# Kernel tuning notes

Measured on AMD Instinct MI355X. Metric: run time of the kernel, lower is better.

Reference implementation:

```python
import jax, jax.numpy as jnp
import numpy as np

B, D_IN, U, M = 8192, 512, 256, 50  # batch, input_size, num_units(=v_size), max_n_msgs


def _w(key, shape, scale=0.02):
    return (jax.random.normal(key, shape, dtype=jnp.float32) * scale)


def setup_inputs() -> dict:
    key = jax.random.key(0)
    ks = jax.random.split(key, 32)
    inp = {
        "X": jax.random.normal(ks[0], (B, D_IN), dtype=jnp.float32),
        "S": jax.random.normal(ks[1], (B, M, U), dtype=jnp.float32),
        "h": jax.random.normal(ks[2], (B, U), dtype=jnp.float32),
        "v": jax.random.normal(ks[3], (B, U), dtype=jnp.float32),
        # attention params
        "W_sa": _w(ks[4], (U, U)), "W_ha": _w(ks[5], (U, U)),
        "b_a": jnp.zeros((U,), jnp.float32), "v_a": _w(ks[6], (U,)),
        # gates
        "W_f": _w(ks[7], (U, U)), "W_hf": _w(ks[8], (U, U)), "b_f": jnp.zeros((U,), jnp.float32),
        "W_o": _w(ks[9], (U, U)), "W_ho": _w(ks[10], (U, U)), "b_o": jnp.zeros((U,), jnp.float32),
        "W_t": _w(ks[11], (U, U)), "W_ht": _w(ks[12], (U, U)), "b_t": jnp.zeros((U,), jnp.float32),
        "W_k": _w(ks[13], (D_IN, U)), "W_hk": _w(ks[14], (U, U)), "W_vk": _w(ks[15], (U, U)), "b_k": jnp.zeros((U,), jnp.float32),
        "W_s": _w(ks[16], (D_IN, U)), "W_hs": _w(ks[17], (U, U)), "b_s": jnp.zeros((U,), jnp.float32),
        "W_v": _w(ks[18], (U, U)), "W_hv": _w(ks[19], (U, U)), "b_v": jnp.zeros((U,), jnp.float32),
    }
    return inp


def reference(X, S, h, v,
              W_sa, W_ha, b_a, v_a,
              W_f, W_hf, b_f,
              W_o, W_ho, b_o,
              W_t, W_ht, b_t,
              W_k, W_hk, W_vk, b_k,
              W_s, W_hs, b_s,
              W_v, W_hv, b_v):
    # additive attention over messages: a [B, M, U]
    a = jnp.tanh(jnp.einsum('bmv,vu->bmu', S, W_sa) + (h @ W_ha + b_a)[:, None, :])
    scores = jnp.einsum('bmu,u->bm', a, v_a)            # [B, M]
    P = jax.nn.softmax(scores, axis=1)                  # [B, M]
    text = jnp.einsum('bm,bmv->bv', P, S)               # [B, U]
    # LSTM-like gates
    F = jax.nn.sigmoid(text @ W_f + h @ W_hf + b_f)
    O = jax.nn.sigmoid(text @ W_o + h @ W_ho + b_o)
    text_new = jnp.tanh(text @ W_t + h @ W_ht + b_t)
    V = F * v + O * text_new                            # [B, U]
    k = jax.nn.sigmoid(X @ W_k + h @ W_hk + V @ W_vk + b_k)
    hx = jnp.tanh(X @ W_s + h @ W_hs + b_s)
    hv = jnp.tanh(V @ W_v + h @ W_hv + b_v)
    H = (1.0 - k) * hv + k * hx                         # [B, U]
    # original returns (H, P, MSINStateTuple(H, V)); new_state.h == H
    return (H, P, V)
```

## Files before the change

### kernel.cpp

```cpp
#include <hip/hip_runtime.h>
#include <cstddef>

typedef __bf16 bf16x8 __attribute__((ext_vector_type(8)));
typedef unsigned short u16x8 __attribute__((ext_vector_type(8)));
typedef float f32x4 __attribute__((ext_vector_type(4)));

#define B_N 8192
#define M_N 50
#define R_N (B_N * M_N)
#define P_OFF ((size_t)B_N * 256)
#define V_OFF ((size_t)B_N * 256 + (size_t)B_N * 50)

__device__ __forceinline__ float bf2f(unsigned short u) {
  return __uint_as_float(((unsigned int)u) << 16);
}
__device__ __forceinline__ unsigned short f2bf(float f) {
  unsigned int u = __float_as_uint(f);
  u += 0x7fffu + ((u >> 16) & 1u);
  return (unsigned short)(u >> 16);
}
__device__ __forceinline__ float fsig(float x) { return 1.f / (1.f + __expf(-x)); }
__device__ __forceinline__ float ftanh(float x) {
  float e = __expf(2.f * x);
  return 1.f - 2.f / (e + 1.f);
}

__device__ __forceinline__ float ld_ext(const void* p, size_t i, bool f32) {
  return f32 ? ((const float*)p)[i] : bf2f(((const unsigned short*)p)[i]);
}

__device__ __forceinline__ void gload_lds16(const void* g, void* l) {
  __builtin_amdgcn_global_load_lds(
      (const __attribute__((address_space(1))) unsigned int*)g,
      (__attribute__((address_space(3))) unsigned int*)l, 16, 0, 0);
}

__device__ __forceinline__ unsigned swz(unsigned b) {
  return b ^ (((b >> 7) & 7u) << 4);
}

__global__ void probe_dtype(const void* __restrict__ X, int* __restrict__ flag) {
  const int lane = threadIdx.x;
  const unsigned short u = ((const unsigned short*)X)[lane * 2];
  const int e = (u >> 7) & 0xff;
  const bool plausible = (e >= 110 && e <= 144) || (u == 0);
  const unsigned long long m = __ballot(plausible);
  if (lane == 0) *flag = (__popcll(m) < 32) ? 1 : 0;
}

struct TJobs {
  const void* src[15];
  unsigned short* dst[15];
  int K[15];
};

__global__ __launch_bounds__(256) void transpose_weights(TJobs jobs, const int* __restrict__ flagp) {
  const bool f32 = *flagp != 0;
  const int z = blockIdx.z;
  const void* __restrict__ src = jobs.src[z];
  unsigned short* __restrict__ dst = jobs.dst[z];
  const int K = jobs.K[z];
  const int k0 = blockIdx.y * 16;
  if (k0 >= K) return;
  const int n0 = blockIdx.x * 16;
  __shared__ __align__(16) unsigned short tile[16][17];
  const int tx = threadIdx.x & 15, ty = threadIdx.x >> 4;
  const size_t sidx = (size_t)(k0 + ty) * 256 + n0 + tx;
  tile[ty][tx] = f32 ? f2bf(((const float*)src)[sidx]) : ((const unsigned short*)src)[sidx];
  __syncthreads();
  dst[(size_t)(n0 + ty) * K + k0 + tx] = tile[tx][ty];
}

struct GJob {
  const void* A[3];
  const unsigned short* Wt[3];
  int K[3];
  int atag[3];
  const void* bias;
  const unsigned short* add;
  unsigned short* out;
  int act;
};
struct GJobs { GJob j[4]; };

__global__ __launch_bounds__(256) void gemm_small(GJobs jobs, const int* __restrict__ flagp) {
  const bool flag32 = *flagp != 0;
  const GJob job = jobs.j[blockIdx.z];
  const int tid = threadIdx.x;
  const int row0 = blockIdx.x * 64;
  const int col0 = blockIdx.y * 128;
  __shared__ __align__(16) unsigned short As[2][64][40];
  __shared__ __align__(16) unsigned short Ws[2][128][40];

  f32x4 acc[2][4];
#pragma unroll
  for (int i = 0; i < 2; ++i)
#pragma unroll
    for (int j = 0; j < 4; ++j) acc[i][j] = (f32x4){0.f, 0.f, 0.f, 0.f};

  const int wave = tid >> 6, lane = tid & 63;
  const int wr = wave >> 1, wc = wave & 1;
  const int quad = lane >> 4, l16 = lane & 15;

  const void* Aseg[3]; const unsigned short* Wseg[3]; int Kseg[3]; bool Fseg[3];
  int nseg = 0, nt = 0, sbeg[4];
  sbeg[0] = 0;
  for (int p = 0; p < 3; ++p) {
    if (job.K[p] == 0) break;
    Aseg[nseg] = job.A[p]; Wseg[nseg] = job.Wt[p]; Kseg[nseg] = job.K[p];
    Fseg[nseg] = (job.atag[p] == 1) || (job.atag[p] == 2 && flag32);
    nt += job.K[p] / 32;
    ++nseg; sbeg[nseg] = nt;
  }

  const int rA = tid >> 2, cA = (tid & 3) * 8;
  const int rW = tid >> 2, cW = (tid & 3) * 8;

  uint4 pa, pw0, pw1;
  float4 fa, fb;
  bool pf32 = false;

  auto issue = [&](int t) {
    int s = 0;
    while (t >= sbeg[s + 1]) ++s;
    const int k0 = (t - sbeg[s]) * 32;
    const int Kp = Kseg[s];
    pf32 = Fseg[s];
    if (pf32) {
      const float* fp = (const float*)Aseg[s] + (size_t)(row0 + rA) * Kp + k0 + cA;
      fa = *(const float4*)fp;
      fb = *(const float4*)(fp + 4);
    } else {
      pa = *(const uint4*)((const unsigned short*)Aseg[s] + (size_t)(row0 + rA) * Kp + k0 + cA);
    }
    pw0 = *(const uint4*)&Wseg[s][(size_t)(col0 + rW) * Kp + k0 + cW];
    pw1 = *(const uint4*)&Wseg[s][(size_t)(col0 + rW + 64) * Kp + k0 + cW];
  };
  auto commit = [&](int buf) {
    if (pf32) {
      u16x8 v;
      v[0] = f2bf(fa.x); v[1] = f2bf(fa.y); v[2] = f2bf(fa.z); v[3] = f2bf(fa.w);
      v[4] = f2bf(fb.x); v[5] = f2bf(fb.y); v[6] = f2bf(fb.z); v[7] = f2bf(fb.w);
      *(u16x8*)&As[buf][rA][cA] = v;
    } else {
      *(uint4*)&As[buf][rA][cA] = pa;
    }
    *(uint4*)&Ws[buf][rW][cW] = pw0;
    *(uint4*)&Ws[buf][rW + 64][cW] = pw1;
  };

  issue(0);
  commit(0);
  __syncthreads();

  int buf = 0;
  for (int t = 0; t < nt; ++t) {
    if (t + 1 < nt) issue(t + 1);
    bf16x8 af[2], bfr[4];
#pragma unroll
    for (int mi = 0; mi < 2; ++mi)
      af[mi] = *(const bf16x8*)&As[buf][wr * 32 + mi * 16 + l16][quad * 8];
#pragma unroll
    for (int ni = 0; ni < 4; ++ni)
      bfr[ni] = *(const bf16x8*)&Ws[buf][wc * 64 + ni * 16 + l16][quad * 8];
#pragma unroll
    for (int mi = 0; mi < 2; ++mi)
#pragma unroll
      for (int ni = 0; ni < 4; ++ni)
        acc[mi][ni] = __builtin_amdgcn_mfma_f32_16x16x32_bf16(af[mi], bfr[ni], acc[mi][ni], 0, 0, 0);
    if (t + 1 < nt) commit(buf ^ 1);
    __syncthreads();
    buf ^= 1;
  }

#pragma unroll
  for (int mi = 0; mi < 2; ++mi) {
#pragma unroll
    for (int ni = 0; ni < 4; ++ni) {
      const int col = col0 + wc * 64 + ni * 16 + l16;
      const float bias = job.bias ? ld_ext(job.bias, col, flag32) : 0.f;
      const int rowb = row0 + wr * 32 + mi * 16 + quad * 4;
#pragma unroll
      for (int r = 0; r < 4; ++r) {
        float v = acc[mi][ni][r] + bias;
        const size_t idx = (size_t)(rowb + r) * 256 + col;
        if (job.add) v += bf2f(job.add[idx]);
        if (job.act == 1) v = fsig(v);
        else if (job.act == 2) v = ftanh(v);
        job.out[idx] = f2bf(v);
      }
    }
  }
}

__global__ __launch_bounds__(512, 4) void attn_scores(
    const void* __restrict__ S,
    const unsigned short* __restrict__ WsaT,
    const unsigned short* __restrict__ hWa,
    const void* __restrict__ v_a,
    float* __restrict__ scores,
    const int* __restrict__ flagp) {
  const bool f32 = *flagp != 0;
  const int tid = threadIdx.x;
  const int r0 = blockIdx.x * 128;

  __shared__ __align__(128) unsigned short As[2 * 128 * 32];
  __shared__ __align__(128) unsigned short Ws[2 * 256 * 32];
  __shared__ float hWs[4][256];
  __shared__ float vas[256];
  __shared__ __align__(16) float red[128][4];

  const int wave = tid >> 6, lane = tid & 63;
  const int wr = wave >> 2, wc = wave & 3;
  const int quad = lane >> 4, l16 = lane & 15;

  const unsigned oA = tid * 16;
  const unsigned lA = swz(oA);
  const unsigned rowA = lA >> 6, slA = (lA >> 4) & 3;
  const size_t gAbase = (size_t)(r0 + rowA) * 256 + slA * 8;
  const size_t gWbase0 = (size_t)rowA * 256 + slA * 8;
  const size_t gWbase1 = (size_t)(rowA + 128) * 256 + slA * 8;

  auto stage = [&](int buf, int k0) {
    char* const aDst = (char*)As + buf * 8192 + (wave << 10);
    char* const wDst0 = (char*)Ws + buf * 16384 + (wave << 10);
    char* const wDst1 = wDst0 + 8192;
    if (f32) {
      const float* fp = (const float*)S + gAbase + k0;
      const float4 a = *(const float4*)fp;
      const float4 b = *(const float4*)(fp + 4);
      u16x8 t;
      t[0] = f2bf(a.x); t[1] = f2bf(a.y); t[2] = f2bf(a.z); t[3] = f2bf(a.w);
      t[4] = f2bf(b.x); t[5] = f2bf(b.y); t[6] = f2bf(b.z); t[7] = f2bf(b.w);
      *(u16x8*)((char*)As + buf * 8192 + oA) = t;
    } else {
      gload_lds16((const unsigned short*)S + gAbase + k0, aDst);
    }
    gload_lds16(WsaT + gWbase0 + k0, wDst0);
    gload_lds16(WsaT + gWbase1 + k0, wDst1);
  };

  f32x4 acc[4][4];
#pragma unroll
  for (int i = 0; i < 4; ++i)
#pragma unroll
    for (int j = 0; j < 4; ++j) acc[i][j] = (f32x4){0.f, 0.f, 0.f, 0.f};

  stage(0, 0);
  const int b_first = r0 / 50;
  for (int i = tid; i < 1024; i += 512) {
    const int j = i >> 8, u = i & 255;
    const int b = b_first + j;
    hWs[j][u] = (b < B_N) ? bf2f(hWa[(size_t)b * 256 + u]) : 0.f;
  }
  if (tid < 256) vas[tid] = ld_ext(v_a, tid, f32);
  __syncthreads();

  int buf = 0;
  for (int t = 0; t < 8; ++t) {
    if (t < 7) stage(buf ^ 1, (t + 1) * 32);
    const char* aB = (const char*)As + buf * 8192;
    const char* wB = (const char*)Ws + buf * 16384;
    bf16x8 af[4], bfr[4];
#pragma unroll
    for (int mi = 0; mi < 4; ++mi) {
      const unsigned lb = (unsigned)(wr * 64 + mi * 16 + l16) * 64 + quad * 16;
      af[mi] = *(const bf16x8*)(aB + swz(lb));
    }
#pragma unroll
    for (int ni = 0; ni < 4; ++ni) {
      const unsigned lb = (unsigned)(wc * 64 + ni * 16 + l16) * 64 + quad * 16;
      bfr[ni] = *(const bf16x8*)(wB + swz(lb));
    }
#pragma unroll
    for (int mi = 0; mi < 4; ++mi)
#pragma unroll
      for (int ni = 0; ni < 4; ++ni)
        acc[mi][ni] = __builtin_amdgcn_mfma_f32_16x16x32_bf16(af[mi], bfr[ni], acc[mi][ni], 0, 0, 0);
    __syncthreads();
    buf ^= 1;
  }

  float ps[4][4];
#pragma unroll
  for (int mi = 0; mi < 4; ++mi) {
#pragma unroll
    for (int r = 0; r < 4; ++r) {
      const int rl = wr * 64 + mi * 16 + quad * 4 + r;
      const int bj = (r0 + rl) / 50 - b_first;
      float s = 0.f;
#pragma unroll
      for (int ni = 0; ni < 4; ++ni) {
        const int col = wc * 64 + ni * 16 + l16;
        s += ftanh(acc[mi][ni][r] + hWs[bj][col]) * vas[col];
      }
      ps[mi][r] = s;
    }
  }
#pragma unroll
  for (int mi = 0; mi < 4; ++mi)
#pragma unroll
    for (int r = 0; r < 4; ++r) {
      float v = ps[mi][r];
      v += __shfl_xor(v, 1);
      v += __shfl_xor(v, 2);
      v += __shfl_xor(v, 4);
      v += __shfl_xor(v, 8);
      if (l16 == 0) red[wr * 64 + mi * 16 + quad * 4 + r][wc] = v;
    }
  __syncthreads();
  if (tid < 128) {
    const float4 rr = *(const float4*)&red[tid][0];
    scores[r0 + tid] = rr.x + rr.y + rr.z + rr.w;
  }
}

__global__ __launch_bounds__(256) void softmax_text(
    const float* __restrict__ scores,
    const void* __restrict__ S,
    float* __restrict__ out,
    unsigned short* __restrict__ text,
    const int* __restrict__ flagp) {
  const bool f32 = *flagp != 0;
  const int tid = threadIdx.x;
  const int wave = tid >> 6, lane = tid & 63;
  const int b = blockIdx.x * 4 + wave;
  __shared__ float Pl[4][64];

  float s = (lane < 50) ? scores[(size_t)b * 50 + lane] : -1e30f;
  float mx = s;
#pragma unroll
  for (int off = 32; off > 0; off >>= 1) mx = fmaxf(mx, __shfl_xor(mx, off));
  float e = (lane < 50) ? __expf(s - mx) : 0.f;
  float sum = e;
#pragma unroll
  for (int off = 32; off > 0; off >>= 1) sum += __shfl_xor(sum, off);
  const float p = e / sum;
  if (lane < 50) out[P_OFF + (size_t)b * 50 + lane] = p;
  Pl[wave][lane] = p;
  __syncthreads();

  float a0 = 0.f, a1 = 0.f, a2 = 0.f, a3 = 0.f;
  const size_t base = (size_t)b * 50 * 256 + lane * 4;
  for (int m = 0; m < 50; ++m) {
    const float pm = Pl[wave][m];
    const size_t ix = base + (size_t)m * 256;
    float s0, s1, s2, s3;
    if (f32) {
      const float4 sv = *(const float4*)((const float*)S + ix);
      s0 = sv.x; s1 = sv.y; s2 = sv.z; s3 = sv.w;
    } else {
      const uint2 raw = *(const uint2*)((const unsigned short*)S + ix);
      s0 = bf2f((unsigned short)(raw.x & 0xffffu));
      s1 = bf2f((unsigned short)(raw.x >> 16));
      s2 = bf2f((unsigned short)(raw.y & 0xffffu));
      s3 = bf2f((unsigned short)(raw.y >> 16));
    }
    a0 += pm * s0; a1 += pm * s1; a2 += pm * s2; a3 += pm * s3;
  }
  uint2 o;
  o.x = (unsigned int)f2bf(a0) | ((unsigned int)f2bf(a1) << 16);
  o.y = (unsigned int)f2bf(a2) | ((unsigned int)f2bf(a3) << 16);
  *(uint2*)&text[(size_t)b * 256 + lane * 4] = o;
}

__global__ __launch_bounds__(256) void v_combine(
    const unsigned short* __restrict__ F, const unsigned short* __restrict__ O,
    const unsigned short* __restrict__ T,
    const void* __restrict__ v, float* __restrict__ out,
    const int* __restrict__ flagp) {
  const bool f32 = *flagp != 0;
  const int i = (blockIdx.x * 256 + threadIdx.x) * 4;
  float v0, v1, v2, v3;
  if (f32) {
    const float4 vv = *(const float4*)((const float*)v + i);
    v0 = vv.x; v1 = vv.y; v2 = vv.z; v3 = vv.w;
  } else {
    const uint2 vr = *(const uint2*)((const unsigned short*)v + i);
    v0 = bf2f((unsigned short)(vr.x & 0xffffu));
    v1 = bf2f((unsigned short)(vr.x >> 16));
    v2 = bf2f((unsigned short)(vr.y & 0xffffu));
    v3 = bf2f((unsigned short)(vr.y >> 16));
  }
  const uint2 Fr = *(const uint2*)&F[i];
  const uint2 Or = *(const uint2*)&O[i];
  const uint2 Tr = *(const uint2*)&T[i];
  float4 o;
  o.x = bf2f((unsigned short)(Fr.x & 0xffffu)) * v0 + bf2f((unsigned short)(Or.x & 0xffffu)) * bf2f((unsigned short)(Tr.x & 0xffffu));
  o.y = bf2f((unsigned short)(Fr.x >> 16))     * v1 + bf2f((unsigned short)(Or.x >> 16))     * bf2f((unsigned short)(Tr.x >> 16));
  o.z = bf2f((unsigned short)(Fr.y & 0xffffu)) * v2 + bf2f((unsigned short)(Or.y & 0xffffu)) * bf2f((unsigned short)(Tr.y & 0xffffu));
  o.w = bf2f((unsigned short)(Fr.y >> 16))     * v3 + bf2f((unsigned short)(Or.y >> 16))     * bf2f((unsigned short)(Tr.y >> 16));
  *(float4*)&out[V_OFF + i] = o;
}

__global__ __launch_bounds__(256) void h_combine(
    const unsigned short* __restrict__ kk, const unsigned short* __restrict__ hv,
    const unsigned short* __restrict__ hx, float* __restrict__ Hout) {
  const int i = (blockIdx.x * 256 + threadIdx.x) * 4;
  const uint2 kr = *(const uint2*)&kk[i];
  const uint2 vr = *(const uint2*)&hv[i];
  const uint2 xr = *(const uint2*)&hx[i];
  const float k0 = bf2f((unsigned short)(kr.x & 0xffffu)), k1 = bf2f((unsigned short)(kr.x >> 16));
  const float k2 = bf2f((unsigned short)(kr.y & 0xffffu)), k3 = bf2f((unsigned short)(kr.y >> 16));
  const float hv0 = bf2f((unsigned short)(vr.x & 0xffffu)), hv1 = bf2f((unsigned short)(vr.x >> 16));
  const float hv2 = bf2f((unsigned short)(vr.y & 0xffffu)), hv3 = bf2f((unsigned short)(vr.y >> 16));
  const float hx0 = bf2f((unsigned short)(xr.x & 0xffffu)), hx1 = bf2f((unsigned short)(xr.x >> 16));
  const float hx2 = bf2f((unsigned short)(xr.y & 0xffffu)), hx3 = bf2f((unsigned short)(xr.y >> 16));
  float4 o;
  o.x = (1.f - k0) * hv0 + k0 * hx0;
  o.y = (1.f - k1) * hv1 + k1 * hx1;
  o.z = (1.f - k2) * hv2 + k2 * hx2;
  o.w = (1.f - k3) * hv3 + k3 * hx3;
  *(float4*)&Hout[i] = o;
}

extern "C" void kernel_launch(void* const* d_in, const int* in_sizes, int n_in,
                              void* d_out, int out_size, void* d_ws, size_t ws_size,
                              hipStream_t stream) {
  const void* X   = d_in[0];
  const void* S   = d_in[1];
  const void* h   = d_in[2];
  const void* v   = d_in[3];
  const void* b_a = d_in[6];
  const void* v_a = d_in[7];
  const void* b_f = d_in[10];
  const void* b_o = d_in[13];
  const void* b_t = d_in[16];
  const void* b_k = d_in[20];
  const void* b_s = d_in[23];
  const void* b_v = d_in[26];

  float* out = (float*)d_out;
  float* out_V = out + V_OFF;

  char* ws = (char*)d_ws;
  int* flag = (int*)ws;
  size_t off = 256;

  const int widx[15] = {4, 5, 8, 9, 11, 12, 14, 15, 17, 18, 19, 21, 22, 24, 25};
  const int wK[15]   = {256, 256, 256, 256, 256, 256, 256, 256, 512, 256, 256, 512, 256, 256, 256};
  TJobs tj;
  unsigned short* wt[15];
  for (int i = 0; i < 15; ++i) {
    wt[i] = (unsigned short*)(ws + off);
    off += (size_t)wK[i] * 256 * 2;
    tj.src[i] = d_in[widx[i]];
    tj.dst[i] = wt[i];
    tj.K[i] = wK[i];
  }
  const unsigned short *WsaT = wt[0], *WhaT = wt[1], *WfT = wt[2], *WhfT = wt[3],
                       *WoT = wt[4], *WhoT = wt[5], *WtT = wt[6], *WhtT = wt[7],
                       *WkT = wt[8], *WhkT = wt[9], *WvkT = wt[10], *WsT = wt[11],
                       *WhsT = wt[12], *WvT = wt[13], *WhvT = wt[14];
  off = (off + 255) & ~(size_t)255;
  const size_t BS = (size_t)B_N * 256 * 2;
  unsigned short* hWa   = (unsigned short*)(ws + off); off += BS;
  float* scores         = (float*)(ws + off);          off += (size_t)R_N * sizeof(float);
  unsigned short* text  = (unsigned short*)(ws + off); off += BS;
  unsigned short* Fb    = (unsigned short*)(ws + off); off += BS;
  unsigned short* Ob    = (unsigned short*)(ws + off); off += BS;
  unsigned short* Tb    = (unsigned short*)(ws + off); off += BS;
  unsigned short* kpre  = (unsigned short*)(ws + off); off += BS;
  unsigned short* hx    = (unsigned short*)(ws + off); off += BS;
  unsigned short* hvpre = (unsigned short*)(ws + off); off += BS;

  probe_dtype<<<1, 64, 0, stream>>>(X, flag);
  transpose_weights<<<dim3(16, 32, 15), 256, 0, stream>>>(tj, flag);

  GJobs jA;
  for (int i = 0; i < 4; ++i) jA.j[i] = GJob{};
  jA.j[0].A[0] = h;  jA.j[0].atag[0] = 2; jA.j[0].Wt[0] = WhaT; jA.j[0].K[0] = 256;
  jA.j[0].bias = b_a; jA.j[0].out = hWa; jA.j[0].act = 0;
  jA.j[1].A[0] = X;  jA.j[1].atag[0] = 2; jA.j[1].Wt[0] = WkT;  jA.j[1].K[0] = 512;
  jA.j[1].A[1] = h;  jA.j[1].atag[1] = 2; jA.j[1].Wt[1] = WhkT; jA.j[1].K[1] = 256;
  jA.j[1].bias = b_k; jA.j[1].out = kpre; jA.j[1].act = 0;
  jA.j[2].A[0] = X;  jA.j[2].atag[0] = 2; jA.j[2].Wt[0] = WsT;  jA.j[2].K[0] = 512;
  jA.j[2].A[1] = h;  jA.j[2].atag[1] = 2; jA.j[2].Wt[1] = WhsT; jA.j[2].K[1] = 256;
  jA.j[2].bias = b_s; jA.j[2].out = hx; jA.j[2].act = 2;
  jA.j[3].A[0] = h;  jA.j[3].atag[0] = 2; jA.j[3].Wt[0] = WhvT; jA.j[3].K[0] = 256;
  jA.j[3].bias = b_v; jA.j[3].out = hvpre; jA.j[3].act = 0;
  gemm_small<<<dim3(128, 2, 4), 256, 0, stream>>>(jA, flag);

  attn_scores<<<dim3(R_N / 128), 512, 0, stream>>>(S, WsaT, hWa, v_a, scores, flag);
  softmax_text<<<dim3(B_N / 4), 256, 0, stream>>>(scores, S, out, text, flag);

  GJobs jB;
  for (int i = 0; i < 4; ++i) jB.j[i] = GJob{};
  jB.j[0].A[0] = text; jB.j[0].atag[0] = 0; jB.j[0].Wt[0] = WfT;  jB.j[0].K[0] = 256;
  jB.j[0].A[1] = h;    jB.j[0].atag[1] = 2; jB.j[0].Wt[1] = WhfT; jB.j[0].K[1] = 256;
  jB.j[0].bias = b_f; jB.j[0].out = Fb; jB.j[0].act = 1;
  jB.j[1].A[0] = text; jB.j[1].atag[0] = 0; jB.j[1].Wt[0] = WoT;  jB.j[1].K[0] = 256;
  jB.j[1].A[1] = h;    jB.j[1].atag[1] = 2; jB.j[1].Wt[1] = WhoT; jB.j[1].K[1] = 256;
  jB.j[1].bias = b_o; jB.j[1].out = Ob; jB.j[1].act = 1;
  jB.j[2].A[0] = text; jB.j[2].atag[0] = 0; jB.j[2].Wt[0] = WtT;  jB.j[2].K[0] = 256;
  jB.j[2].A[1] = h;    jB.j[2].atag[1] = 2; jB.j[2].Wt[1] = WhtT; jB.j[2].K[1] = 256;
  jB.j[2].bias = b_t; jB.j[2].out = Tb; jB.j[2].act = 2;
  gemm_small<<<dim3(128, 2, 3), 256, 0, stream>>>(jB, flag);

  v_combine<<<dim3(B_N * 256 / 1024), 256, 0, stream>>>(Fb, Ob, Tb, v, out, flag);

  GJobs jC;
  for (int i = 0; i < 4; ++i) jC.j[i] = GJob{};
  jC.j[0].A[0] = out_V; jC.j[0].atag[0] = 1; jC.j[0].Wt[0] = WvkT; jC.j[0].K[0] = 256;
  jC.j[0].add = kpre; jC.j[0].out = kpre; jC.j[0].act = 1;
  jC.j[1].A[0] = out_V; jC.j[1].atag[0] = 1; jC.j[1].Wt[0] = WvT;  jC.j[1].K[0] = 256;
  jC.j[1].add = hvpre; jC.j[1].out = hvpre; jC.j[1].act = 2;
  gemm_small<<<dim3(128, 2, 2), 256, 0, stream>>>(jC, flag);

  h_combine<<<dim3(B_N * 256 / 1024), 256, 0, stream>>>(kpre, hvpre, hx, out);
}
```

Measured before the change: 863.5 us.

## Fuse attention scores, softmax and text reduction into one per-batch kernel

Replaces the separate attention-score GEMM kernel and the softmax/text kernel with a single kernel that handles one batch row (50 messages, padded to 64) per block. The S tile stays resident in LDS as bf16, so the weighted sum for text reuses it instead of reading S from global memory a second time, and the scores buffer round trip is removed. In exchange each block computes a 64x256 tile with 14 padded rows, and every block reloads the full W_sa matrix (8192 blocks instead of 3200), which raises weight traffic and lowers MFMA utilisation.

Result: no change. 858.2 us (-0.6%).

```diff
diff --git a/kernel.cpp b/kernel.cpp
--- a/kernel.cpp
+++ b/kernel.cpp
@@ -35,8 +35,8 @@
       (__attribute__((address_space(3))) unsigned int*)l, 16, 0, 0);
 }
 
-__device__ __forceinline__ unsigned swz(unsigned b) {
-  return b ^ (((b >> 7) & 7u) << 4);
+__device__ __forceinline__ unsigned swz(unsigned a) {
+  return a ^ (((a >> 7) & 7u) << 4);
 }
 
 __global__ void probe_dtype(const void* __restrict__ X, int* __restrict__ flag) {
@@ -193,175 +193,144 @@
   }
 }
 
-__global__ __launch_bounds__(512, 4) void attn_scores(
+__global__ __launch_bounds__(512, 4) void attn_fused(
     const void* __restrict__ S,
     const unsigned short* __restrict__ WsaT,
     const unsigned short* __restrict__ hWa,
     const void* __restrict__ v_a,
-    float* __restrict__ scores,
-    const int* __restrict__ flagp) {
-  const bool f32 = *flagp != 0;
-  const int tid = threadIdx.x;
-  const int r0 = blockIdx.x * 128;
-
-  __shared__ __align__(128) unsigned short As[2 * 128 * 32];
-  __shared__ __align__(128) unsigned short Ws[2 * 256 * 32];
-  __shared__ float hWs[4][256];
-  __shared__ float vas[256];
-  __shared__ __align__(16) float red[128][4];
-
-  const int wave = tid >> 6, lane = tid & 63;
-  const int wr = wave >> 2, wc = wave & 3;
-  const int quad = lane >> 4, l16 = lane & 15;
-
-  const unsigned oA = tid * 16;
-  const unsigned lA = swz(oA);
-  const unsigned rowA = lA >> 6, slA = (lA >> 4) & 3;
-  const size_t gAbase = (size_t)(r0 + rowA) * 256 + slA * 8;
-  const size_t gWbase0 = (size_t)rowA * 256 + slA * 8;
-  const size_t gWbase1 = (size_t)(rowA + 128) * 256 + slA * 8;
-
-  auto stage = [&](int buf, int k0) {
-    char* const aDst = (char*)As + buf * 8192 + (wave << 10);
-    char* const wDst0 = (char*)Ws + buf * 16384 + (wave << 10);
-    char* const wDst1 = wDst0 + 8192;
-    if (f32) {
-      const float* fp = (const float*)S + gAbase + k0;
-      const float4 a = *(const float4*)fp;
-      const float4 b = *(const float4*)(fp + 4);
-      u16x8 t;
-      t[0] = f2bf(a.x); t[1] = f2bf(a.y); t[2] = f2bf(a.z); t[3] = f2bf(a.w);
-      t[4] = f2bf(b.x); t[5] = f2bf(b.y); t[6] = f2bf(b.z); t[7] = f2bf(b.w);
-      *(u16x8*)((char*)As + buf * 8192 + oA) = t;
-    } else {
-      gload_lds16((const unsigned short*)S + gAbase + k0, aDst);
-    }
-    gload_lds16(WsaT + gWbase0 + k0, wDst0);
-    gload_lds16(WsaT + gWbase1 + k0, wDst1);
-  };
-
-  f32x4 acc[4][4];
-#pragma unroll
-  for (int i = 0; i < 4; ++i)
-#pragma unroll
-    for (int j = 0; j < 4; ++j) acc[i][j] = (f32x4){0.f, 0.f, 0.f, 0.f};
-
-  stage(0, 0);
-  const int b_first = r0 / 50;
-  for (int i = tid; i < 1024; i += 512) {
-    const int j = i >> 8, u = i & 255;
-    const int b = b_first + j;
-    hWs[j][u] = (b < B_N) ? bf2f(hWa[(size_t)b * 256 + u]) : 0.f;
-  }
-  if (tid < 256) vas[tid] = ld_ext(v_a, tid, f32);
-  __syncthreads();
-
-  int buf = 0;
-  for (int t = 0; t < 8; ++t) {
-    if (t < 7) stage(buf ^ 1, (t + 1) * 32);
-    const char* aB = (const char*)As + buf * 8192;
-    const char* wB = (const char*)Ws + buf * 16384;
-    bf16x8 af[4], bfr[4];
-#pragma unroll
-    for (int mi = 0; mi < 4; ++mi) {
-      const unsigned lb = (unsigned)(wr * 64 + mi * 16 + l16) * 64 + quad * 16;
-      af[mi] = *(const bf16x8*)(aB + swz(lb));
-    }
-#pragma unroll
-    for (int ni = 0; ni < 4; ++ni) {
-      const unsigned lb = (unsigned)(wc * 64 + ni * 16 + l16) * 64 + quad * 16;
-      bfr[ni] = *(const bf16x8*)(wB + swz(lb));
-    }
-#pragma unroll
-    for (int mi = 0; mi < 4; ++mi)
-#pragma unroll
-      for (int ni = 0; ni < 4; ++ni)
-        acc[mi][ni] = __builtin_amdgcn_mfma_f32_16x16x32_bf16(af[mi], bfr[ni], acc[mi][ni], 0, 0, 0);
-    __syncthreads();
-    buf ^= 1;
-  }
-
-  float ps[4][4];
-#pragma unroll
-  for (int mi = 0; mi < 4; ++mi) {
-#pragma unroll
-    for (int r = 0; r < 4; ++r) {
-      const int rl = wr * 64 + mi * 16 + quad * 4 + r;
-      const int bj = (r0 + rl) / 50 - b_first;
-      float s = 0.f;
-#pragma unroll
-      for (int ni = 0; ni < 4; ++ni) {
-        const int col = wc * 64 + ni * 16 + l16;
-        s += ftanh(acc[mi][ni][r] + hWs[bj][col]) * vas[col];
-      }
-      ps[mi][r] = s;
-    }
-  }
-#pragma unroll
-  for (int mi = 0; mi < 4; ++mi)
-#pragma unroll
-    for (int r = 0; r < 4; ++r) {
-      float v = ps[mi][r];
-      v += __shfl_xor(v, 1);
-      v += __shfl_xor(v, 2);
-      v += __shfl_xor(v, 4);
-      v += __shfl_xor(v, 8);
-      if (l16 == 0) red[wr * 64 + mi * 16 + quad * 4 + r][wc] = v;
-    }
-  __syncthreads();
-  if (tid < 128) {
-    const float4 rr = *(const float4*)&red[tid][0];
-    scores[r0 + tid] = rr.x + rr.y + rr.z + rr.w;
-  }
-}
-
-__global__ __launch_bounds__(256) void softmax_text(
-    const float* __restrict__ scores,
-    const void* __restrict__ S,
     float* __restrict__ out,
     unsigned short* __restrict__ text,
     const int* __restrict__ flagp) {
   const bool f32 = *flagp != 0;
   const int tid = threadIdx.x;
+  const int b0 = blockIdx.x;
+  const size_t srow0 = (size_t)b0 * 50;
+
+  __shared__ __align__(128) unsigned short Sl[8 * 64 * 32];
+  __shared__ __align__(128) unsigned short Wl[2 * 256 * 32];
+  __shared__ float hWs[256];
+  __shared__ float vas[256];
+  __shared__ __align__(16) float red[64][4];
+  __shared__ float Pl[64];
+
   const int wave = tid >> 6, lane = tid & 63;
-  const int b = blockIdx.x * 4 + wave;
-  __shared__ float Pl[4][64];
-
-  float s = (lane < 50) ? scores[(size_t)b * 50 + lane] : -1e30f;
-  float mx = s;
-#pragma unroll
-  for (int off = 32; off > 0; off >>= 1) mx = fmaxf(mx, __shfl_xor(mx, off));
-  float e = (lane < 50) ? __expf(s - mx) : 0.f;
-  float sum = e;
-#pragma unroll
-  for (int off = 32; off > 0; off >>= 1) sum += __shfl_xor(sum, off);
-  const float p = e / sum;
-  if (lane < 50) out[P_OFF + (size_t)b * 50 + lane] = p;
-  Pl[wave][lane] = p;
+  const int wr = wave >> 2, wc = wave & 3;
+  const int quad = lane >> 4, l16 = lane & 15;
+
+  const unsigned cS = (unsigned)tid * 16;
+  const unsigned lS = swz(cS);
+  const unsigned rowS = lS >> 6;
+  const unsigned eS = (lS & 63) >> 1;
+  const size_t gS = (srow0 + (rowS < 50 ? rowS : 49)) * 256 + eS;
+
+  const unsigned c0 = (unsigned)tid * 16, c1 = c0 + 8192;
+  const unsigned l0 = swz(c0), l1 = swz(c1);
+  const size_t gW0 = (size_t)(l0 >> 6) * 256 + ((l0 & 63) >> 1);
+  const size_t gW1 = (size_t)(l1 >> 6) * 256 + ((l1 & 63) >> 1);
+
+  auto stageS = [&](int t) {
+    if (wave < 4) {
+      if (f32) {
+        const float* fp = (const float*)S + gS + t * 32;
+        const float4 a = *(const float4*)fp;
+        const float4 b = *(const float4*)(fp + 4);
+        u16x8 v;
+        v[0] = f2bf(a.x); v[1] = f2bf(a.y); v[2] = f2bf(a.z); v[3] = f2bf(a.w);
+        v[4] = f2bf(b.x); v[5] = f2bf(b.y); v[6] = f2bf(b.z); v[7] = f2bf(b.w);
+        *(u16x8*)((char*)Sl + t * 4096 + cS) = v;
+      } else {
+        gload_lds16((const unsigned short*)S + gS + t * 32,
+                    (char*)Sl + t * 4096 + (wave << 10));
+      }
+    }
+  };
+  auto stageW = [&](int t, int buf) {
+    char* base = (char*)Wl + buf * 16384;
+    gload_lds16(WsaT + gW0 + t * 32, base + (wave << 10));
+    gload_lds16(WsaT + gW1 + t * 32, base + 8192 + (wave << 10));
+  };
+
+  f32x4 acc[2][4];
+#pragma unroll
+  for (int i = 0; i < 2; ++i)
+#pragma unroll
+    for (int j = 0; j < 4; ++j) acc[i][j] = (f32x4){0.f, 0.f, 0.f, 0.f};
+
+  stageS(0);
+  stageW(0, 0);
+  if (tid < 256) {
+    hWs[tid] = bf2f(hWa[(size_t)b0 * 256 + tid]);
+    vas[tid] = ld_ext(v_a, tid, f32);
+  }
   __syncthreads();
 
-  float a0 = 0.f, a1 = 0.f, a2 = 0.f, a3 = 0.f;
-  const size_t base = (size_t)b * 50 * 256 + lane * 4;
-  for (int m = 0; m < 50; ++m) {
-    const float pm = Pl[wave][m];
-    const size_t ix = base + (size_t)m * 256;
-    float s0, s1, s2, s3;
-    if (f32) {
-      const float4 sv = *(const float4*)((const float*)S + ix);
-      s0 = sv.x; s1 = sv.y; s2 = sv.z; s3 = sv.w;
-    } else {
-      const uint2 raw = *(const uint2*)((const unsigned short*)S + ix);
-      s0 = bf2f((unsigned short)(raw.x & 0xffffu));
-      s1 = bf2f((unsigned short)(raw.x >> 16));
-      s2 = bf2f((unsigned short)(raw.y & 0xffffu));
-      s3 = bf2f((unsigned short)(raw.y >> 16));
-    }
-    a0 += pm * s0; a1 += pm * s1; a2 += pm * s2; a3 += pm * s3;
-  }
-  uint2 o;
-  o.x = (unsigned int)f2bf(a0) | ((unsigned int)f2bf(a1) << 16);
-  o.y = (unsigned int)f2bf(a2) | ((unsigned int)f2bf(a3) << 16);
-  *(uint2*)&text[(size_t)b * 256 + lane * 4] = o;
+  for (int t = 0; t < 8; ++t) {
+    if (t < 7) { stageS(t + 1); stageW(t + 1, (t + 1) & 1); }
+    const char* sl = (const char*)Sl + t * 4096;
+    const char* wl = (const char*)Wl + (t & 1) * 16384;
+    bf16x8 af[2], bfr[4];
+#pragma unroll
+    for (int mi = 0; mi < 2; ++mi)
+      af[mi] = *(const bf16x8*)(sl + swz((unsigned)(wr * 32 + mi * 16 + l16) * 64 + quad * 16));
+#pragma unroll
+    for (int ni = 0; ni < 4; ++ni)
+      bfr[ni] = *(const bf16x8*)(wl + swz((unsigned)(wc * 64 + ni * 16 + l16) * 64 + quad * 16));
+#pragma unroll
+    for (int mi = 0; mi < 2; ++mi)
+#pragma unroll
+      for (int ni = 0; ni < 4; ++ni)
+        acc[mi][ni] = __builtin_amdgcn_mfma_f32_16x16x32_bf16(af[mi], bfr[ni], acc[mi][ni], 0, 0, 0);
+    __syncthreads();
+  }
+
+#pragma unroll
+  for (int mi = 0; mi < 2; ++mi) {
+#pragma unroll
+    for (int r = 0; r < 4; ++r) {
+      const int rl = wr * 32 + mi * 16 + quad * 4 + r;
+      float s = 0.f;
+#pragma unroll
+      for (int ni = 0; ni < 4; ++ni) {
+        const int col = wc * 64 + ni * 16 + l16;
+        s += ftanh(acc[mi][ni][r] + hWs[col]) * vas[col];
+      }
+      s += __shfl_xor(s, 1);
+      s += __shfl_xor(s, 2);
+      s += __shfl_xor(s, 4);
+      s += __shfl_xor(s, 8);
+      if (l16 == 0) red[rl][wc] = s;
+    }
+  }
+  __syncthreads();
+
+  if (tid < 64) {
+    const float4 rr = *(const float4*)&red[tid][0];
+    const float sc = rr.x + rr.y + rr.z + rr.w;
+    float sv = (tid < 50) ? sc : -1e30f;
+    float mx = sv;
+#pragma unroll
+    for (int off = 32; off > 0; off >>= 1) mx = fmaxf(mx, __shfl_xor(mx, off));
+    float e = (tid < 50) ? __expf(sv - mx) : 0.f;
+    float sum = e;
+#pragma unroll
+    for (int off = 32; off > 0; off >>= 1) sum += __shfl_xor(sum, off);
+    const float p = e / sum;
+    Pl[tid] = p;
+    if (tid < 50) out[P_OFF + (size_t)b0 * 50 + tid] = p;
+  }
+  __syncthreads();
+
+  if (tid < 256) {
+    const int t = tid >> 5;
+    const unsigned bc = (unsigned)(tid & 31) * 2;
+    float a = 0.f;
+#pragma unroll 10
+    for (int m = 0; m < 50; ++m) {
+      const unsigned off = (unsigned)t * 4096 + swz((unsigned)m * 64 + bc);
+      a += Pl[m] * bf2f(*(const unsigned short*)((const char*)Sl + off));
+    }
+    text[(size_t)b0 * 256 + tid] = f2bf(a);
+  }
 }
 
 __global__ __launch_bounds__(256) void v_combine(
@@ -455,7 +424,6 @@
   off = (off + 255) & ~(size_t)255;
   const size_t BS = (size_t)B_N * 256 * 2;
   unsigned short* hWa   = (unsigned short*)(ws + off); off += BS;
-  float* scores         = (float*)(ws + off);          off += (size_t)R_N * sizeof(float);
   unsigned short* text  = (unsigned short*)(ws + off); off += BS;
   unsigned short* Fb    = (unsigned short*)(ws + off); off += BS;
   unsigned short* Ob    = (unsigned short*)(ws + off); off += BS;
@@ -481,8 +449,7 @@
   jA.j[3].bias = b_v; jA.j[3].out = hvpre; jA.j[3].act = 0;
   gemm_small<<<dim3(128, 2, 4), 256, 0, stream>>>(jA, flag);
 
-  attn_scores<<<dim3(R_N / 128), 512, 0, stream>>>(S, WsaT, hWa, v_a, scores, flag);
-  softmax_text<<<dim3(B_N / 4), 256, 0, stream>>>(scores, S, out, text, flag);
+  attn_fused<<<dim3(B_N), 512, 0, stream>>>(S, WsaT, hWa, v_a, out, text, flag);
 
   GJobs jB;
   for (int i = 0; i < 4; ++i) jB.j[i] = GJob{};
```
